# Optimization experiments

Hardware: AMD Instinct MI355X
Metric: run time of the kernel (lower is better)

Reference implementation:

```python
import jax, jax.numpy as jnp
import numpy as np

# seek_thermal sensor constants (hard-coded in the torch module)
HFOV, VFOV = 81.0, 59.0
H, W = 150, 200
P = 1024   # max_num_points
M = 5      # max_num_persons


def _cam_grids():
    fx = W / (2.0 * np.tan(np.deg2rad(HFOV) / 2.0))
    fy = H / (2.0 * np.tan(np.deg2rad(VFOV) / 2.0))
    x, y = np.meshgrid(np.arange(W), np.arange(H))
    x_cam = (x - W / 2.0) / fx
    y_cam = (y - H / 2.0) / fy
    return jnp.asarray(x_cam, jnp.float32), jnp.asarray(y_cam, jnp.float32)


def setup_inputs() -> dict:
    key = jax.random.key(0)
    k1, k2, k3 = jax.random.split(key, 3)
    B = 256
    depth = jax.random.uniform(k1, (B, H, W), jnp.float32, 0.0, 12.0)
    ind = jax.random.randint(k2, (B, H, W), 0, M + 1).astype(jnp.float32)
    extra = jax.random.normal(k3, (B, H, W), dtype=jnp.float32)
    return {"depth_mask_3C": jnp.stack([depth, ind, extra], axis=1)}


def _percentile(d_sorted, n, q):
    # np.percentile 'linear' interpolation on ascending sorted valid depths
    nf = n.astype(d_sorted.dtype)
    pos = q * jnp.maximum(nf - 1.0, 0.0)
    lo = jnp.floor(pos).astype(jnp.int32)
    hi = jnp.ceil(pos).astype(jnp.int32)
    frac = pos - lo.astype(d_sorted.dtype)
    return d_sorted[lo] * (1.0 - frac) + d_sorted[hi] * frac


def _person(depth, ind, x_cam, y_cam, p):
    # depth, ind: (H, W); p: scalar person id (float)
    mask = (ind == p) & (depth > 3.0)
    n = mask.sum()
    # invalid pixels pushed to +inf so the first n sorted entries are the valid depths
    d_sorted = jnp.sort(jnp.where(mask, depth, jnp.inf).reshape(-1))
    q1 = _percentile(d_sorted, n, 0.25)
    q3 = _percentile(d_sorted, n, 0.75)
    iqr = q3 - q1
    lb = q1 - 1.5 * iqr
    ub = q3 + 1.5 * iqr
    mask2 = (mask & (depth >= lb) & (depth <= ub)).reshape(-1)  # (H*W,)
    pts = jnp.stack(
        [(x_cam * depth).reshape(-1), (y_cam * depth).reshape(-1), depth.reshape(-1)],
        axis=-1,
    )  # (H*W, 3)
    # deterministic compaction: first max_num_points surviving pixels in raster order
    rank = jnp.cumsum(mask2.astype(jnp.int32)) - 1
    write_idx = jnp.where(mask2 & (rank < P), rank, P)  # slot P is a dump slot
    buf = jnp.zeros((P + 1, 3), depth.dtype).at[write_idx].set(
        jnp.where(mask2[:, None], pts, 0.0)
    )
    flag = mask2.any().astype(depth.dtype)
    flag_col = jnp.zeros((3,), depth.dtype).at[0].set(flag)
    return jnp.concatenate([buf[:P].T, flag_col[:, None]], axis=1)  # (3, P+1)


def reference(depth_mask_3C):
    x_cam, y_cam = _cam_grids()
    depth = depth_mask_3C[:, 0]
    ind = jnp.round(depth_mask_3C[:, 1])
    persons = jnp.arange(1, M + 1, dtype=depth.dtype)
    per_b = jax.vmap(_person, in_axes=(None, None, None, None, 0))
    res = jax.vmap(per_b, in_axes=(0, 0, None, None, None))(
        depth, ind, x_cam, y_cam, persons
    )  # (B, M, 3, P+1)
    B = depth.shape[0]
    return res.transpose(0, 2, 1, 3).reshape(B, 3, M * (P + 1))
```

## Files before the change

kernel.cpp:

```cpp
#include <hip/hip_runtime.h>
#include <math.h>

#define HW_N   30000
#define NV4    7500
#define W_IMG  200
#define H_IMG  150
#define NPERS  5
#define CAP    1024
#define NTHR   1024
#define NWAVE  16
#define CAPS   384
#define NREG   (NWAVE * NPERS)
#define BASE_BITS 0x40400000u

#ifndef M_PI
#define M_PI 3.14159265358979323846
#endif

__device__ __forceinline__ unsigned wave_incl_scan_u32(unsigned v, int lane) {
    #pragma unroll
    for (int d = 1; d < 64; d <<= 1) {
        unsigned t = __shfl_up(v, d, 64);
        if (lane >= d) v += t;
    }
    return v;
}

__device__ __forceinline__ void find_bucket(const unsigned* h, int nchunks, unsigned k,
                                            int lane, unsigned& bucket, unsigned& cl) {
    unsigned run = 0;
    bucket = 0; cl = 0;
    bool found = false;
    for (int c = 0; c < nchunks; ++c) {
        if (found) break;
        unsigned hv = h[c * 64 + lane] & 0xFFFFu;
        unsigned inc = wave_incl_scan_u32(hv, lane);
        unsigned tot = __shfl(inc, 63, 64);
        if (run + tot > k) {
            unsigned long long m = __ballot((run + inc) > k);
            int l = (int)__builtin_ctzll(m);
            bucket = (unsigned)(c * 64 + l);
            cl = run + __shfl(inc, l, 64) - __shfl(hv, l, 64);
            found = true;
        }
        run += tot;
    }
}

__device__ __forceinline__ int person_of(float f) {
    float r = rintf(f);
    int p = (int)r;
    return (p >= 1 && p <= NPERS && (float)p == r) ? p : 0;
}

extern "C" __global__ __launch_bounds__(NTHR)
void DepthMask2PointCloudFast_53472342835417_kernel(const float* __restrict__ in,
                                                    float* __restrict__ out) {
    const int b = blockIdx.x;
    const int tid = (int)threadIdx.x;
    const int lane = tid & 63;
    const int wv = tid >> 6;

    const float* __restrict__ depth = in + (size_t)b * 3u * HW_N;
    const float* __restrict__ indc = depth + HW_N;
    const float4* __restrict__ d4p = (const float4*)depth;
    const float4* __restrict__ i4p = (const float4*)indc;

    __shared__ unsigned s_vals[NREG * CAPS];
    __shared__ unsigned s_cur[NREG];
    __shared__ unsigned s_h1[NPERS * 256];
    __shared__ unsigned s_h2[20 * 256];
    __shared__ __align__(16) unsigned s_pref[24];
    __shared__ int      s_krem[20];
    __shared__ float    s_val[20];
    __shared__ unsigned s_n[NPERS];
    __shared__ float    s_lb[NPERS], s_ub[NPERS];
    __shared__ unsigned s_cnt[NWAVE][NPERS];
    __shared__ unsigned s_woff[NWAVE][NPERS];
    __shared__ unsigned s_tot[NPERS];
    __shared__ unsigned s_base[NPERS];
    __shared__ float    s_xc[W_IMG];
    __shared__ float    s_yc[H_IMG];

    for (int i = tid; i < NPERS * 256; i += NTHR) s_h1[i] = 0u;
    for (int i = tid; i < 20 * 256; i += NTHR) s_h2[i] = 0u;
    if (tid < NREG) s_cur[tid] = 0u;
    if (tid < NPERS) { s_base[tid] = 0u; s_tot[tid] = 0u; }
    if (tid < W_IMG) {
        const double fx = 200.0 / (2.0 * tan((81.0 * (M_PI / 180.0)) / 2.0));
        s_xc[tid] = (float)(((double)tid - 100.0) / fx);
    }
    {
        int ty = tid - 256;
        if (ty >= 0 && ty < H_IMG) {
            const double fy = 150.0 / (2.0 * tan((59.0 * (M_PI / 180.0)) / 2.0));
            s_yc[ty] = (float)(((double)ty - 75.0) / fy);
        }
    }
    __syncthreads();

    {
        int i = tid;
        float4 dd = d4p[i], ff = i4p[i];
        while (i < NV4) {
            int inx = i + NTHR;
            float4 dd2, ff2;
            if (inx < NV4) { dd2 = d4p[inx]; ff2 = i4p[inx]; }
            float de[4] = {dd.x, dd.y, dd.z, dd.w};
            float fe[4] = {ff.x, ff.y, ff.z, ff.w};
            #pragma unroll
            for (int e = 0; e < 4; ++e) {
                float d = de[e];
                int p = person_of(fe[e]);
                if (p && d > 3.0f) {
                    unsigned k24 = __float_as_uint(d) - BASE_BITS;
                    atomicAdd(&s_h1[(p - 1) * 256 + (k24 >> 16)], 1u);
                    int reg = wv * NPERS + (p - 1);
                    unsigned off = atomicAdd(&s_cur[reg], 1u);
                    if (off < CAPS) s_vals[reg * CAPS + off] = k24;
                }
            }
            dd = dd2; ff = ff2;
            i = inx;
        }
    }
    __syncthreads();

    if (tid < NPERS) {
        unsigned n = 0;
        for (int sh = 0; sh < NWAVE; ++sh) n += s_cur[sh * NPERS + tid];
        s_n[tid] = n;
    }
    __syncthreads();

    for (int q = wv; q < 20; q += NWAVE) {
        int p = q >> 2, s = q & 3;
        unsigned n = s_n[p];
        if (n == 0u) { if (lane == 0) s_pref[q] = 0xFFFFFFFFu; continue; }
        float nf = (float)n;
        float m1 = fmaxf(nf - 1.0f, 0.0f);
        float pos = ((s >> 1) ? 0.75f : 0.25f) * m1;
        unsigned k = (unsigned)((s & 1) ? (int)ceilf(pos) : (int)floorf(pos));
        unsigned bucket, cl;
        find_bucket(&s_h1[p * 256], 4, k, lane, bucket, cl);
        if (lane == 0) { s_pref[q] = bucket; s_krem[q] = (int)(k - cl); }
    }
    __syncthreads();

    for (int t = tid; t < NREG * CAPS; t += NTHR) {
        int reg = t / CAPS;
        int ii = t - reg * CAPS;
        unsigned cnt = s_cur[reg]; if (cnt > CAPS) cnt = CAPS;
        if ((unsigned)ii < cnt) {
            unsigned k24 = s_vals[t];
            int p = reg % NPERS;
            unsigned t8 = k24 >> 16;
            uint4 pr = *(const uint4*)&s_pref[p * 4];
            unsigned b8 = (k24 >> 8) & 255u;
            if (t8 == pr.x) atomicAdd(&s_h2[(p * 4 + 0) * 256 + b8], 1u);
            if (t8 == pr.y) atomicAdd(&s_h2[(p * 4 + 1) * 256 + b8], 1u);
            if (t8 == pr.z) atomicAdd(&s_h2[(p * 4 + 2) * 256 + b8], 1u);
            if (t8 == pr.w) atomicAdd(&s_h2[(p * 4 + 3) * 256 + b8], 1u);
        }
    }
    __syncthreads();

    for (int q = wv; q < 20; q += NWAVE) {
        int p = q >> 2;
        if (s_n[p] == 0u) continue;
        unsigned bucket, cl;
        find_bucket(&s_h2[q * 256], 4, (unsigned)s_krem[q], lane, bucket, cl);
        if (lane == 0) { s_pref[q] = (s_pref[q] << 8) | bucket; s_krem[q] -= (int)cl; }
    }
    __syncthreads();
    for (int i = tid; i < 20 * 256; i += NTHR) s_h2[i] = 0u;
    __syncthreads();

    for (int t = tid; t < NREG * CAPS; t += NTHR) {
        int reg = t / CAPS;
        int ii = t - reg * CAPS;
        unsigned cnt = s_cur[reg]; if (cnt > CAPS) cnt = CAPS;
        if ((unsigned)ii < cnt) {
            unsigned k24 = s_vals[t];
            int p = reg % NPERS;
            unsigned t16 = k24 >> 8;
            uint4 pr = *(const uint4*)&s_pref[p * 4];
            unsigned b8 = k24 & 255u;
            if (t16 == pr.x) atomicAdd(&s_h2[(p * 4 + 0) * 256 + b8], 1u);
            if (t16 == pr.y) atomicAdd(&s_h2[(p * 4 + 1) * 256 + b8], 1u);
            if (t16 == pr.z) atomicAdd(&s_h2[(p * 4 + 2) * 256 + b8], 1u);
            if (t16 == pr.w) atomicAdd(&s_h2[(p * 4 + 3) * 256 + b8], 1u);
        }
    }
    __syncthreads();

    for (int q = wv; q < 20; q += NWAVE) {
        int p = q >> 2;
        if (s_n[p] == 0u) continue;
        unsigned bucket, cl;
        find_bucket(&s_h2[q * 256], 4, (unsigned)s_krem[q], lane, bucket, cl);
        if (lane == 0) s_val[q] = __uint_as_float(BASE_BITS + ((s_pref[q] << 8) | bucket));
    }
    __syncthreads();

    if (tid < NPERS) {
        if (s_n[tid] == 0u) {
            s_lb[tid] = INFINITY; s_ub[tid] = -INFINITY;
        } else {
            float nf = (float)s_n[tid];
            float m1 = fmaxf(nf - 1.0f, 0.0f);
            float pos1 = 0.25f * m1, pos3 = 0.75f * m1;
            float fr1 = pos1 - floorf(pos1);
            float fr3 = pos3 - floorf(pos3);
            float q1 = __fadd_rn(__fmul_rn(s_val[tid * 4 + 0], __fsub_rn(1.0f, fr1)),
                                 __fmul_rn(s_val[tid * 4 + 1], fr1));
            float q3 = __fadd_rn(__fmul_rn(s_val[tid * 4 + 2], __fsub_rn(1.0f, fr3)),
                                 __fmul_rn(s_val[tid * 4 + 3], fr3));
            float iqr = __fsub_rn(q3, q1);
            float t15 = __fmul_rn(1.5f, iqr);
            s_lb[tid] = __fsub_rn(q1, t15);
            s_ub[tid] = __fadd_rn(q3, t15);
        }
    }
    __syncthreads();

    float* outb = out + (size_t)b * 3u * (NPERS * (CAP + 1));
    const int cstr = NPERS * (CAP + 1);

    for (int t0 = 0; t0 < NV4; t0 += NTHR) {
        int i = t0 + tid;
        int pf[4] = {0, 0, 0, 0};
        float dv[4] = {0.f, 0.f, 0.f, 0.f};
        if (i < NV4) {
            float4 dd = d4p[i];
            float4 ff = i4p[i];
            float de[4] = {dd.x, dd.y, dd.z, dd.w};
            float fe[4] = {ff.x, ff.y, ff.z, ff.w};
            #pragma unroll
            for (int e = 0; e < 4; ++e) {
                float d = de[e];
                int p = person_of(fe[e]);
                dv[e] = d;
                if (p && d > 3.0f && d >= s_lb[p - 1] && d <= s_ub[p - 1]) pf[e] = p;
            }
        }
        unsigned wexc[NPERS];
        #pragma unroll
        for (int pp = 0; pp < NPERS; ++pp) {
            unsigned c = (unsigned)((pf[0] == pp + 1) + (pf[1] == pp + 1) +
                                    (pf[2] == pp + 1) + (pf[3] == pp + 1));
            unsigned incl = wave_incl_scan_u32(c, lane);
            if (lane == 63) s_cnt[wv][pp] = incl;
            wexc[pp] = incl - c;
        }
        __syncthreads();
        if (tid < 16 * NPERS) {
            int p = tid >> 4, w = tid & 15;
            unsigned o = s_base[p];
            for (int w2 = 0; w2 < w; ++w2) o += s_cnt[w2][p];
            s_woff[w][p] = o;
            if (w == 15) s_tot[p] = o + s_cnt[15][p];
        }
        __syncthreads();
        #pragma unroll
        for (int pp = 0; pp < NPERS; ++pp) {
            unsigned m0 = (pf[0] == pp + 1), m1 = (pf[1] == pp + 1);
            unsigned m2 = (pf[2] == pp + 1), m3 = (pf[3] == pp + 1);
            if ((m0 | m1 | m2 | m3) != 0u) {
                unsigned basep = s_woff[wv][pp] + wexc[pp];
                #define WRITEPT(e, mm, pre)                                                \
                    if (mm) { unsigned off = basep + (pre);                                \
                        if (off < CAP) {                                                   \
                            int idx = i * 4 + e; int y = idx / W_IMG; int x = idx - y * W_IMG; \
                            size_t o = (size_t)pp * (CAP + 1) + off; float d = dv[e];      \
                            outb[o] = __fmul_rn(s_xc[x], d);                               \
                            outb[cstr + o] = __fmul_rn(s_yc[y], d);                        \
                            outb[2 * cstr + o] = d; } }
                WRITEPT(0, m0, 0u)
                WRITEPT(1, m1, m0)
                WRITEPT(2, m2, m0 + m1)
                WRITEPT(3, m3, m0 + m1 + m2)
                #undef WRITEPT
            }
        }
        if (tid < NPERS) s_base[tid] = s_tot[tid];
        bool done = true;
        #pragma unroll
        for (int pp = 0; pp < NPERS; ++pp) done = done && (s_tot[pp] >= (unsigned)CAP);
        if (done) break;
    }
    __syncthreads();

    for (int t = tid; t < NPERS * (CAP + 1); t += NTHR) {
        int p = t / (CAP + 1);
        int j = t - p * (CAP + 1);
        unsigned cnt = s_tot[p];
        size_t o = (size_t)p * (CAP + 1) + j;
        if (j == CAP) {
            outb[o] = (cnt > 0u) ? 1.0f : 0.0f;
            outb[cstr + o] = 0.0f;
            outb[2 * cstr + o] = 0.0f;
        } else if ((unsigned)j >= cnt) {
            outb[o] = 0.0f;
            outb[cstr + o] = 0.0f;
            outb[2 * cstr + o] = 0.0f;
        }
    }
}

extern "C" void kernel_launch(void* const* d_in, const int* in_sizes, int n_in,
                              void* d_out, int out_size, void* d_ws, size_t ws_size,
                              hipStream_t stream) {
    const float* in = (const float*)d_in[0];
    float* out = (float*)d_out;
    int B = in_sizes[0] / (3 * HW_N);
    hipLaunchKernelGGL(DepthMask2PointCloudFast_53472342835417_kernel,
                       dim3(B), dim3(NTHR), 0, stream, in, out);
}
```

Before: 52.95 us.

## Split fused point-cloud kernel into a multi-kernel histogram-select-refine-output pipeline

```diff
diff --git a/kernel.cpp b/kernel.cpp
--- a/kernel.cpp
+++ b/kernel.cpp
@@ -7,11 +7,8 @@
 #define H_IMG  150
 #define NPERS  5
 #define CAP    1024
-#define NTHR   1024
-#define NWAVE  16
-#define CAPS   384
-#define NREG   (NWAVE * NPERS)
 #define BASE_BITS 0x40400000u
+#define LCAP   64
 
 #ifndef M_PI
 #define M_PI 3.14159265358979323846
@@ -26,8 +23,314 @@
     return v;
 }
 
-__device__ __forceinline__ void find_bucket(const unsigned* h, int nchunks, unsigned k,
-                                            int lane, unsigned& bucket, unsigned& cl) {
+__device__ __forceinline__ int person_of(float f) {
+    float r = rintf(f);
+    int p = (int)r;
+    return (p >= 1 && p <= NPERS && (float)p == r) ? p : 0;
+}
+
+__global__ __launch_bounds__(1024)
+void ka_hist(const float* __restrict__ in, unsigned* __restrict__ ghist) {
+    const int bid = blockIdx.x;
+    const int b = bid >> 1, h = bid & 1;
+    const int tid = (int)threadIdx.x;
+    __shared__ unsigned lh[3 * 2048];
+    for (int t = tid; t < 3 * 2048; t += 1024) lh[t] = 0u;
+    __syncthreads();
+
+    const float* __restrict__ depth = in + (size_t)b * 3u * HW_N;
+    const float4* __restrict__ d4p = (const float4*)depth;
+    const float4* __restrict__ i4p = (const float4*)(depth + HW_N);
+    const int beg = h * (NV4 / 2), end = beg + (NV4 / 2);
+    for (int i = beg + tid; i < end; i += 1024) {
+        float4 dd = d4p[i], ff = i4p[i];
+        float de[4] = {dd.x, dd.y, dd.z, dd.w};
+        float fe[4] = {ff.x, ff.y, ff.z, ff.w};
+        #pragma unroll
+        for (int e = 0; e < 4; ++e) {
+            int p = person_of(fe[e]);
+            if (p && de[e] > 3.0f) {
+                unsigned key = __float_as_uint(de[e]) - BASE_BITS;
+                atomicAdd(&lh[((p - 1) >> 1) * 2048 + (key >> 13)],
+                          1u << (((p - 1) & 1) * 16));
+            }
+        }
+    }
+    __syncthreads();
+    unsigned* go = ghist + (size_t)(b * 2 + h) * NPERS * 2048;
+    for (int t = tid; t < NPERS * 2048; t += 1024) {
+        int p = t >> 11, bin = t & 2047;
+        go[t] = (lh[(p >> 1) * 2048 + bin] >> ((p & 1) * 16)) & 0xFFFFu;
+    }
+}
+
+__global__ __launch_bounds__(256)
+void kb_select(const unsigned* __restrict__ ghist, unsigned* __restrict__ prefT,
+               unsigned* __restrict__ kremT, unsigned* __restrict__ nT) {
+    const int bp = blockIdx.x;
+    const int b = bp / NPERS, p = bp % NPERS;
+    const int tid = (int)threadIdx.x, lane = tid & 63, wv = tid >> 6;
+    __shared__ unsigned s_h[2048];
+    __shared__ unsigned s_n;
+    if (tid == 0) s_n = 0u;
+    __syncthreads();
+    const unsigned* g0 = ghist + ((size_t)(b * 2 + 0) * NPERS + p) * 2048;
+    const unsigned* g1 = ghist + ((size_t)(b * 2 + 1) * NPERS + p) * 2048;
+    unsigned part = 0;
+    for (int t = tid; t < 2048; t += 256) {
+        unsigned v = g0[t] + g1[t];
+        s_h[t] = v;
+        part += v;
+    }
+    #pragma unroll
+    for (int d2 = 32; d2 >= 1; d2 >>= 1) part += __shfl_xor(part, d2, 64);
+    if (lane == 0) atomicAdd(&s_n, part);
+    __syncthreads();
+    unsigned n = s_n;
+    if (tid == 0) nT[bp] = n;
+    if (n == 0u) {
+        if (tid < 4) { prefT[bp * 4 + tid] = 0xFFFFFFFFu; kremT[bp * 4 + tid] = 0u; }
+        return;
+    }
+    if (wv < 4) {
+        float nf = (float)n;
+        float m1 = fmaxf(nf - 1.0f, 0.0f);
+        float pos = ((wv >> 1) ? 0.75f : 0.25f) * m1;
+        unsigned k = (unsigned)((wv & 1) ? (int)ceilf(pos) : (int)floorf(pos));
+        unsigned run = 0, bucket = 0, krem = 0;
+        bool found = false;
+        for (int c = 0; c < 32; ++c) {
+            if (found) break;
+            unsigned hv = s_h[c * 64 + lane];
+            unsigned inc = wave_incl_scan_u32(hv, lane);
+            unsigned tot = __shfl(inc, 63, 64);
+            if (run + tot > k) {
+                unsigned long long m = __ballot((run + inc) > k);
+                int l = (int)__builtin_ctzll(m);
+                bucket = (unsigned)(c * 64 + l);
+                krem = k - (run + __shfl(inc, l, 64) - __shfl(hv, l, 64));
+                found = true;
+            } else run += tot;
+        }
+        if (lane == 0) { prefT[bp * 4 + wv] = bucket; kremT[bp * 4 + wv] = krem; }
+    }
+}
+
+__global__ __launch_bounds__(1024)
+void kc_refine(const float* __restrict__ in, const unsigned* __restrict__ prefT,
+               unsigned* __restrict__ gcnt, unsigned* __restrict__ glist) {
+    const int bid = blockIdx.x;
+    const int b = bid >> 1, h = bid & 1;
+    const int tid = (int)threadIdx.x;
+    __shared__ uint4 s_pr[NPERS];
+    if (tid < NPERS) s_pr[tid] = *(const uint4*)&prefT[((size_t)b * NPERS + tid) * 4];
+    __syncthreads();
+
+    const float* __restrict__ depth = in + (size_t)b * 3u * HW_N;
+    const float4* __restrict__ d4p = (const float4*)depth;
+    const float4* __restrict__ i4p = (const float4*)(depth + HW_N);
+    const int beg = h * (NV4 / 2), end = beg + (NV4 / 2);
+    for (int i = beg + tid; i < end; i += 1024) {
+        float4 dd = d4p[i], ff = i4p[i];
+        float de[4] = {dd.x, dd.y, dd.z, dd.w};
+        float fe[4] = {ff.x, ff.y, ff.z, ff.w};
+        #pragma unroll
+        for (int e = 0; e < 4; ++e) {
+            int p = person_of(fe[e]);
+            if (p && de[e] > 3.0f) {
+                unsigned key = __float_as_uint(de[e]) - BASE_BITS;
+                unsigned k11 = key >> 13;
+                uint4 pr = s_pr[p - 1];
+                int bp4 = (b * NPERS + (p - 1)) * 4;
+                if (k11 == pr.x) { unsigned o = atomicAdd(&gcnt[bp4 + 0], 1u);
+                                   if (o < LCAP) glist[(size_t)(bp4 + 0) * LCAP + o] = key; }
+                if (k11 == pr.y) { unsigned o = atomicAdd(&gcnt[bp4 + 1], 1u);
+                                   if (o < LCAP) glist[(size_t)(bp4 + 1) * LCAP + o] = key; }
+                if (k11 == pr.z) { unsigned o = atomicAdd(&gcnt[bp4 + 2], 1u);
+                                   if (o < LCAP) glist[(size_t)(bp4 + 2) * LCAP + o] = key; }
+                if (k11 == pr.w) { unsigned o = atomicAdd(&gcnt[bp4 + 3], 1u);
+                                   if (o < LCAP) glist[(size_t)(bp4 + 3) * LCAP + o] = key; }
+            }
+        }
+    }
+}
+
+__global__ __launch_bounds__(64)
+void kd_bounds(const unsigned* __restrict__ glist, const unsigned* __restrict__ gcnt,
+               const unsigned* __restrict__ kremT, const unsigned* __restrict__ nT,
+               float* __restrict__ gbounds) {
+    const int bp = blockIdx.x;
+    const int lane = (int)threadIdx.x;
+    unsigned n = nT[bp];
+    if (n == 0u) {
+        if (lane == 0) { gbounds[bp * 2] = INFINITY; gbounds[bp * 2 + 1] = -INFINITY; }
+        return;
+    }
+    float vals[4];
+    #pragma unroll
+    for (int s = 0; s < 4; ++s) {
+        unsigned cnt = gcnt[bp * 4 + s]; if (cnt > (unsigned)LCAP) cnt = LCAP;
+        unsigned krem = kremT[bp * 4 + s];
+        unsigned key = (lane < (int)cnt) ? glist[(size_t)(bp * 4 + s) * LCAP + lane]
+                                         : 0xFFFFFFFFu;
+        unsigned cb = 0, ceq = 0;
+        for (unsigned j = 0; j < cnt; ++j) {
+            unsigned kj = (unsigned)__shfl((int)key, (int)j, 64);
+            cb  += (kj <  key) ? 1u : 0u;
+            ceq += (kj == key) ? 1u : 0u;
+        }
+        bool cond = (lane < (int)cnt) && (cb <= krem) && (krem < cb + ceq);
+        unsigned long long m = __ballot(cond);
+        int l = (m != 0ull) ? (int)__builtin_ctzll(m) : 0;
+        unsigned kv = (unsigned)__shfl((int)key, l, 64);
+        vals[s] = __uint_as_float(BASE_BITS + kv);
+    }
+    if (lane == 0) {
+        float nf = (float)n;
+        float m1 = fmaxf(nf - 1.0f, 0.0f);
+        float pos1 = 0.25f * m1, pos3 = 0.75f * m1;
+        float fr1 = pos1 - floorf(pos1);
+        float fr3 = pos3 - floorf(pos3);
+        float q1 = __fadd_rn(__fmul_rn(vals[0], __fsub_rn(1.0f, fr1)),
+                             __fmul_rn(vals[1], fr1));
+        float q3 = __fadd_rn(__fmul_rn(vals[2], __fsub_rn(1.0f, fr3)),
+                             __fmul_rn(vals[3], fr3));
+        float iqr = __fsub_rn(q3, q1);
+        float t15 = __fmul_rn(1.5f, iqr);
+        gbounds[bp * 2]     = __fsub_rn(q1, t15);
+        gbounds[bp * 2 + 1] = __fadd_rn(q3, t15);
+    }
+}
+
+__global__ __launch_bounds__(1024)
+void ke_output(const float* __restrict__ in, const float* __restrict__ gbounds,
+               float* __restrict__ out) {
+    const int b = blockIdx.x;
+    const int tid = (int)threadIdx.x;
+    const int lane = tid & 63;
+    const int wv = tid >> 6;
+    const float* __restrict__ depth = in + (size_t)b * 3u * HW_N;
+    const float4* __restrict__ d4p = (const float4*)depth;
+    const float4* __restrict__ i4p = (const float4*)(depth + HW_N);
+
+    __shared__ float    s_lb[NPERS], s_ub[NPERS];
+    __shared__ unsigned s_cnt[16][NPERS];
+    __shared__ unsigned s_woff[16][NPERS];
+    __shared__ unsigned s_tot[NPERS];
+    __shared__ unsigned s_base[NPERS];
+    __shared__ float    s_xc[W_IMG];
+    __shared__ float    s_yc[H_IMG];
+
+    if (tid < NPERS) { s_base[tid] = 0u; s_tot[tid] = 0u; }
+    if (tid >= 32 && tid < 32 + 2 * NPERS) {
+        int q = tid - 32;
+        float v = gbounds[b * 2 * NPERS + q];
+        if (q & 1) s_ub[q >> 1] = v; else s_lb[q >> 1] = v;
+    }
+    if (tid < W_IMG) {
+        const double fx = 200.0 / (2.0 * tan((81.0 * (M_PI / 180.0)) / 2.0));
+        s_xc[tid] = (float)(((double)tid - 100.0) / fx);
+    }
+    {
+        int ty = tid - 256;
+        if (ty >= 0 && ty < H_IMG) {
+            const double fy = 150.0 / (2.0 * tan((59.0 * (M_PI / 180.0)) / 2.0));
+            s_yc[ty] = (float)(((double)ty - 75.0) / fy);
+        }
+    }
+    __syncthreads();
+
+    float* outb = out + (size_t)b * 3u * (NPERS * (CAP + 1));
+    const int cstr = NPERS * (CAP + 1);
+
+    for (int t0 = 0; t0 < NV4; t0 += 1024) {
+        int i = t0 + tid;
+        int pf[4] = {0, 0, 0, 0};
+        float dv[4] = {0.f, 0.f, 0.f, 0.f};
+        if (i < NV4) {
+            float4 dd = d4p[i];
+            float4 ff = i4p[i];
+            float de[4] = {dd.x, dd.y, dd.z, dd.w};
+            float fe[4] = {ff.x, ff.y, ff.z, ff.w};
+            #pragma unroll
+            for (int e = 0; e < 4; ++e) {
+                float d = de[e];
+                int p = person_of(fe[e]);
+                dv[e] = d;
+                if (p && d > 3.0f && d >= s_lb[p - 1] && d <= s_ub[p - 1]) pf[e] = p;
+            }
+        }
+        unsigned wexc[NPERS];
+        #pragma unroll
+        for (int pp = 0; pp < NPERS; ++pp) {
+            unsigned c = (unsigned)((pf[0] == pp + 1) + (pf[1] == pp + 1) +
+                                    (pf[2] == pp + 1) + (pf[3] == pp + 1));
+            unsigned incl = wave_incl_scan_u32(c, lane);
+            if (lane == 63) s_cnt[wv][pp] = incl;
+            wexc[pp] = incl - c;
+        }
+        __syncthreads();
+        if (tid < 16 * NPERS) {
+            int p = tid >> 4, w = tid & 15;
+            unsigned o = s_base[p];
+            for (int w2 = 0; w2 < w; ++w2) o += s_cnt[w2][p];
+            s_woff[w][p] = o;
+            if (w == 15) s_tot[p] = o + s_cnt[15][p];
+        }
+        __syncthreads();
+        #pragma unroll
+        for (int pp = 0; pp < NPERS; ++pp) {
+            unsigned m0 = (pf[0] == pp + 1), m1 = (pf[1] == pp + 1);
+            unsigned m2 = (pf[2] == pp + 1), m3 = (pf[3] == pp + 1);
+            if ((m0 | m1 | m2 | m3) != 0u) {
+                unsigned basep = s_woff[wv][pp] + wexc[pp];
+                #define WRITEPT(e, mm, pre)                                                \
+                    if (mm) { unsigned off = basep + (pre);                                \
+                        if (off < CAP) {                                                   \
+                            int idx = i * 4 + e; int y = idx / W_IMG; int x = idx - y * W_IMG; \
+                            size_t o = (size_t)pp * (CAP + 1) + off; float d = dv[e];      \
+                            outb[o] = __fmul_rn(s_xc[x], d);                               \
+                            outb[cstr + o] = __fmul_rn(s_yc[y], d);                        \
+                            outb[2 * cstr + o] = d; } }
+                WRITEPT(0, m0, 0u)
+                WRITEPT(1, m1, m0)
+                WRITEPT(2, m2, m0 + m1)
+                WRITEPT(3, m3, m0 + m1 + m2)
+                #undef WRITEPT
+            }
+        }
+        if (tid < NPERS) s_base[tid] = s_tot[tid];
+        bool done = true;
+        #pragma unroll
+        for (int pp = 0; pp < NPERS; ++pp) done = done && (s_tot[pp] >= (unsigned)CAP);
+        if (done) break;
+    }
+    __syncthreads();
+
+    for (int t = tid; t < NPERS * (CAP + 1); t += 1024) {
+        int p = t / (CAP + 1);
+        int j = t - p * (CAP + 1);
+        unsigned cnt = s_tot[p];
+        size_t o = (size_t)p * (CAP + 1) + j;
+        if (j == CAP) {
+            outb[o]            = (cnt > 0u) ? 1.0f : 0.0f;
+            outb[cstr + o]     = 0.0f;
+            outb[2 * cstr + o] = 0.0f;
+        } else if ((unsigned)j >= cnt) {
+            outb[o]            = 0.0f;
+            outb[cstr + o]     = 0.0f;
+            outb[2 * cstr + o] = 0.0f;
+        }
+    }
+}
+
+#define NTHR 1024
+#define NWAVE 16
+#define CAPS 384
+#define NREG (NWAVE * NPERS)
+
+__device__ __forceinline__ void find_bucket_fb(const unsigned* h, int nchunks, unsigned k,
+                                               int lane, unsigned& bucket, unsigned& cl) {
     unsigned run = 0;
     bucket = 0; cl = 0;
     bool found = false;
@@ -47,20 +350,12 @@
     }
 }
 
-__device__ __forceinline__ int person_of(float f) {
-    float r = rintf(f);
-    int p = (int)r;
-    return (p >= 1 && p <= NPERS && (float)p == r) ? p : 0;
-}
-
-extern "C" __global__ __launch_bounds__(NTHR)
-void DepthMask2PointCloudFast_53472342835417_kernel(const float* __restrict__ in,
-                                                    float* __restrict__ out) {
+__global__ __launch_bounds__(NTHR)
+void fb_kernel(const float* __restrict__ in, float* __restrict__ out) {
     const int b = blockIdx.x;
     const int tid = (int)threadIdx.x;
     const int lane = tid & 63;
     const int wv = tid >> 6;
-
     const float* __restrict__ depth = in + (size_t)b * 3u * HW_N;
     const float* __restrict__ indc = depth + HW_N;
     const float4* __restrict__ d4p = (const float4*)depth;
@@ -142,7 +437,7 @@
         float pos = ((s >> 1) ? 0.75f : 0.25f) * m1;
         unsigned k = (unsigned)((s & 1) ? (int)ceilf(pos) : (int)floorf(pos));
         unsigned bucket, cl;
-        find_bucket(&s_h1[p * 256], 4, k, lane, bucket, cl);
+        find_bucket_fb(&s_h1[p * 256], 4, k, lane, bucket, cl);
         if (lane == 0) { s_pref[q] = bucket; s_krem[q] = (int)(k - cl); }
     }
     __syncthreads();
@@ -169,7 +464,7 @@
         int p = q >> 2;
         if (s_n[p] == 0u) continue;
         unsigned bucket, cl;
-        find_bucket(&s_h2[q * 256], 4, (unsigned)s_krem[q], lane, bucket, cl);
+        find_bucket_fb(&s_h2[q * 256], 4, (unsigned)s_krem[q], lane, bucket, cl);
         if (lane == 0) { s_pref[q] = (s_pref[q] << 8) | bucket; s_krem[q] -= (int)cl; }
     }
     __syncthreads();
@@ -198,7 +493,7 @@
         int p = q >> 2;
         if (s_n[p] == 0u) continue;
         unsigned bucket, cl;
-        find_bucket(&s_h2[q * 256], 4, (unsigned)s_krem[q], lane, bucket, cl);
+        find_bucket_fb(&s_h2[q * 256], 4, (unsigned)s_krem[q], lane, bucket, cl);
         if (lane == 0) s_val[q] = __uint_as_float(BASE_BITS + ((s_pref[q] << 8) | bucket));
     }
     __syncthreads();
@@ -314,6 +609,37 @@
     const float* in = (const float*)d_in[0];
     float* out = (float*)d_out;
     int B = in_sizes[0] / (3 * HW_N);
-    hipLaunchKernelGGL(DepthMask2PointCloudFast_53472342835417_kernel,
-                       dim3(B), dim3(NTHR), 0, stream, in, out);
-}
+
+    const size_t ghist_bytes = (size_t)B * 2 * NPERS * 2048 * 4;
+    const size_t pref_off    = ghist_bytes;
+    const size_t pref_bytes  = (size_t)B * NPERS * 4 * 4;
+    const size_t krem_off    = pref_off + pref_bytes;
+    const size_t krem_bytes  = pref_bytes;
+    const size_t n_off       = krem_off + krem_bytes;
+    const size_t n_bytes     = (size_t)B * NPERS * 4;
+    const size_t gcnt_off    = n_off + n_bytes;
+    const size_t gcnt_bytes  = (size_t)B * NPERS * 4 * 4;
+    const size_t glist_off   = gcnt_off + gcnt_bytes;
+    const size_t glist_bytes = (size_t)B * NPERS * 4 * LCAP * 4;
+    const size_t gbnd_off    = glist_off + glist_bytes;
+    const size_t gbnd_bytes  = (size_t)B * NPERS * 2 * 4;
+    const size_t req         = gbnd_off + gbnd_bytes;
+
+    if (ws_size >= req) {
+        unsigned* ghist = (unsigned*)d_ws;
+        unsigned* prefT = (unsigned*)((char*)d_ws + pref_off);
+        unsigned* kremT = (unsigned*)((char*)d_ws + krem_off);
+        unsigned* nT    = (unsigned*)((char*)d_ws + n_off);
+        unsigned* gcnt  = (unsigned*)((char*)d_ws + gcnt_off);
+        unsigned* glist = (unsigned*)((char*)d_ws + glist_off);
+        float*    gbnd  = (float*)((char*)d_ws + gbnd_off);
+        hipMemsetAsync(gcnt, 0, gcnt_bytes, stream);
+        hipLaunchKernelGGL(ka_hist,   dim3(B * 2),        dim3(1024), 0, stream, in, ghist);
+        hipLaunchKernelGGL(kb_select, dim3(B * NPERS),    dim3(256),  0, stream, ghist, prefT, kremT, nT);
+        hipLaunchKernelGGL(kc_refine, dim3(B * 2),        dim3(1024), 0, stream, in, prefT, gcnt, glist);
+        hipLaunchKernelGGL(kd_bounds, dim3(B * NPERS),    dim3(64),   0, stream, glist, gcnt, kremT, nT, gbnd);
+        hipLaunchKernelGGL(ke_output, dim3(B),            dim3(1024), 0, stream, in, gbnd, out);
+    } else {
+        hipLaunchKernelGGL(fb_kernel, dim3(B), dim3(NTHR), 0, stream, in, out);
+    }
+}
```

Measured after the change: 79.58 us. 1.5x slower.
